# Kernel tuning notes

Measured on AMD Instinct MI355X. Metric: run time of the kernel, lower is better.

Reference implementation:

```python
import jax, jax.numpy as jnp
import numpy as np

N = 16000
E = 128000
IN_DIM = 512
H1 = 4096
H2 = 1024
OUT_DIM = 64


def setup_inputs() -> dict:
    key = jax.random.key(0)
    ks = jax.random.split(key, 8)
    x = jax.random.normal(ks[0], (N, IN_DIM), dtype=jnp.float32)
    edge_index = jax.random.randint(ks[1], (2, E), 0, N, dtype=jnp.int64)

    def glorot(k, fan_in, fan_out):
        lim = float(np.sqrt(6.0 / (fan_in + fan_out)))
        return jax.random.uniform(k, (fan_in, fan_out), jnp.float32, -lim, lim)

    # PyG SAGEConv: out = lin_l(mean_j x_j) + lin_r(x); lin_l has bias, lin_r does not.
    params = {
        'W1l': glorot(ks[2], IN_DIM, H1), 'b1': jnp.zeros((H1,), jnp.float32),
        'W1r': glorot(ks[3], IN_DIM, H1),
        'W2l': glorot(ks[4], H1, H2), 'b2': jnp.zeros((H2,), jnp.float32),
        'W2r': glorot(ks[5], H1, H2),
        'W3l': glorot(ks[6], H2, OUT_DIM), 'b3': jnp.zeros((OUT_DIM,), jnp.float32),
        'W3r': glorot(ks[7], H2, OUT_DIM),
    }
    return {'x': x, 'edge_index': edge_index, **params}


def _sage_conv(x, src, dst, Wl, b, Wr):
    # mean-aggregate neighbor features at dst, then linear; plus root transform
    agg = jax.ops.segment_sum(x[src], dst, num_segments=N)          # [N, F_in]
    cnt = jax.ops.segment_sum(jnp.ones((src.shape[0],), x.dtype), dst, num_segments=N)
    mean = agg / jnp.maximum(cnt, 1.0)[:, None]
    return mean @ Wl + b + x @ Wr


def reference(x, edge_index, W1l, b1, W1r, W2l, b2, W2r, W3l, b3, W3r):
    src, dst = edge_index[0], edge_index[1]
    h = jax.nn.relu(_sage_conv(x, src, dst, W1l, b1, W1r))   # dropout is identity in eval
    h = jax.nn.relu(_sage_conv(h, src, dst, W2l, b2, W2r))
    h = _sage_conv(h, src, dst, W3l, b3, W3r)
    return jax.nn.log_softmax(h, axis=1)
```

## Files before the change

### kernel.cpp

```cpp
#include <hip/hip_runtime.h>
#include <stdint.h>

typedef __bf16 bf16x8 __attribute__((ext_vector_type(8)));
typedef float  f32x4  __attribute__((ext_vector_type(4)));
typedef float  f32x16 __attribute__((ext_vector_type(16)));
typedef unsigned short u16x8 __attribute__((ext_vector_type(8)));
typedef const void __attribute__((address_space(1))) gv_t;
typedef void __attribute__((address_space(3))) sv_t;

static __device__ __forceinline__ unsigned short f2bf(float f) {
  unsigned u = __float_as_uint(f);
  u += 0x7fffu + ((u >> 16) & 1u);
  return (unsigned short)(u >> 16);
}
static __device__ __forceinline__ float bf2f(unsigned short h) {
  return __uint_as_float(((unsigned)h) << 16);
}
static __device__ __forceinline__ void gload16(const void* g, void* l) {
  __builtin_amdgcn_global_load_lds((gv_t*)g, (sv_t*)l, 16, 0, 0);
}

__global__ void k_sentinel(float* out, int n, float val) {
  int t = blockIdx.x * 256 + threadIdx.x;
  if (t < n) out[t] = val;
}

static __device__ __forceinline__ void transW_tile(const float* W, unsigned short* Wt,
                                                   int K, int N, int ld, int kofs,
                                                   int n0, int k0, float (*tile)[33]) {
  int tx = threadIdx.x & 31, ty = threadIdx.x >> 5;
#pragma unroll
  for (int r = 0; r < 4; ++r)
    tile[ty + r * 8][tx] = W[(size_t)(k0 + ty + r * 8) * N + n0 + tx];
  __syncthreads();
#pragma unroll
  for (int r = 0; r < 4; ++r)
    Wt[(size_t)(n0 + ty + r * 8) * ld + kofs + k0 + tx] = f2bf(tile[tx][ty + r * 8]);
}

__global__ void k_prep(const float4* __restrict__ x, ushort4* __restrict__ xm,
                       const float* W1l, const float* W1r, const float* W2l,
                       const float* W2r, const float* W3l, const float* W3r,
                       unsigned short* W1t, unsigned short* W2t, unsigned short* W3t,
                       int* deg, int Nn) {
  __shared__ float tile[32][33];
  int bid = blockIdx.x;
  if (bid < 8000) {
    int t = bid * 256 + threadIdx.x;
    int row = t >> 7, c = t & 127;
    float4 v = x[t];
    xm[(size_t)row * 256 + c] = make_ushort4(f2bf(v.x), f2bf(v.y), f2bf(v.z), f2bf(v.w));
    return;
  }
  bid -= 8000;
  if (bid < 2048) {
    transW_tile(W1r, W1t, 512, 4096, 1024, 0, (bid & 127) * 32, (bid >> 7) * 32, tile);
    return;
  }
  bid -= 2048;
  if (bid < 2048) {
    transW_tile(W1l, W1t, 512, 4096, 1024, 512, (bid & 127) * 32, (bid >> 7) * 32, tile);
    return;
  }
  bid -= 2048;
  if (bid < 4096) {
    transW_tile(W2l, W2t, 4096, 1024, 4096, 0, (bid & 31) * 32, (bid >> 5) * 32, tile);
    return;
  }
  bid -= 4096;
  if (bid < 4096) {
    transW_tile(W2r, W2t + (size_t)1024 * 4096, 4096, 1024, 4096, 0, (bid & 31) * 32,
                (bid >> 5) * 32, tile);
    return;
  }
  bid -= 4096;
  if (bid < 64) {
    transW_tile(W3l, W3t, 1024, 64, 1024, 0, (bid & 1) * 32, (bid >> 1) * 32, tile);
    return;
  }
  bid -= 64;
  if (bid < 64) {
    transW_tile(W3r, W3t + (size_t)64 * 1024, 1024, 64, 1024, 0, (bid & 1) * 32,
                (bid >> 1) * 32, tile);
    return;
  }
  bid -= 64;
  {
    int t = bid * 256 + threadIdx.x;
    if (t < Nn) deg[t] = 0;
  }
}

static __device__ __forceinline__ int detect_i64(const int* ei) {
  __shared__ int sflag;
  if (threadIdx.x < 64) {
    int bad = 0;
#pragma unroll
    for (int j = 0; j < 4; ++j) bad |= ei[2 * (threadIdx.x * 4 + j) + 1];
    unsigned long long m = __ballot(bad != 0);
    if (threadIdx.x == 0) sflag = (m == 0ull) ? 1 : 0;
  }
  __syncthreads();
  return sflag;
}

__global__ void k_degree(const int* ei, int E, int* deg) {
  int f = detect_i64(ei);
  int t = blockIdx.x * 256 + threadIdx.x;
  if (t < E) {
    int d = f ? ei[2 * (E + t)] : ei[E + t];
    atomicAdd(&deg[d], 1);
  }
}
__global__ void k_scan(const int* deg, int* rp, int* cur, int n) {
  __shared__ int ssum[256];
  int t = threadIdx.x;
  int chunk = (n + 255) >> 8;
  int lo = t * chunk, hi = min(lo + chunk, n);
  int s = 0;
  for (int i = lo; i < hi; ++i) s += deg[i];
  ssum[t] = s;
  __syncthreads();
  if (t == 0) {
    int run = 0;
    for (int i = 0; i < 256; ++i) { int v = ssum[i]; ssum[i] = run; run += v; }
  }
  __syncthreads();
  int run = ssum[t];
  for (int i = lo; i < hi; ++i) { rp[i] = run; cur[i] = run; run += deg[i]; }
  if (t == 255) rp[n] = run;
}
__global__ void k_fill(const int* ei, int E, int* cur, int* col) {
  int f = detect_i64(ei);
  int t = blockIdx.x * 256 + threadIdx.x;
  if (t < E) {
    int s = f ? ei[2 * t] : ei[t];
    int d = f ? ei[2 * (E + t)] : ei[E + t];
    int p = atomicAdd(&cur[d], 1);
    col[p] = s;
  }
}

__global__ void k_agg(unsigned short* __restrict__ xm, const int* __restrict__ rp,
                      const int* __restrict__ col) {
  int i = blockIdx.x;
  int s = rp[i], e = rp[i + 1];
  float inv = 1.0f / (float)max(e - s, 1);
  int f8 = threadIdx.x & 63;
  int p = threadIdx.x >> 6;
  const u16x8* xm8 = (const u16x8*)xm;
  float acc[8] = {0.f, 0.f, 0.f, 0.f, 0.f, 0.f, 0.f, 0.f};
  for (int n = s + p; n < e; n += 4) {
    u16x8 v = xm8[(size_t)col[n] * 128 + f8];
#pragma unroll
    for (int j = 0; j < 8; ++j) acc[j] += bf2f(v[j]);
  }
  __shared__ float red[3][64][8];
  if (p > 0) {
#pragma unroll
    for (int j = 0; j < 8; ++j) red[p - 1][f8][j] = acc[j];
  }
  __syncthreads();
  if (p == 0) {
    u16x8 o;
#pragma unroll
    for (int j = 0; j < 8; ++j) {
      float v = (acc[j] + red[0][f8][j] + red[1][f8][j] + red[2][f8][j]) * inv;
      o[j] = f2bf(v);
    }
    ((u16x8*)xm)[(size_t)i * 128 + 64 + f8] = o;
  }
}

#define XCD_SWZ(bnShift_)                                                             \
  const int nwg = gridDim.x;                                                          \
  const int q8 = nwg >> 3, r8 = nwg & 7;                                              \
  const int xcd = blockIdx.x & 7, idx = blockIdx.x >> 3;                              \
  const int wg = (xcd < r8 ? xcd * (q8 + 1) : r8 * (q8 + 1) + (xcd - r8) * q8) + idx; \
  const int bn = wg & ((1 << (bnShift_)) - 1);                                        \
  const int bm = wg >> (bnShift_);

#define VMCNT(NUM) asm volatile("s_waitcnt vmcnt(" #NUM ")" ::: "memory")

#define STAGE_A(BUF, I, K0)                                            \
  gload16(Ap + (size_t)((I) * 64 + rsub) * K + (K0) + sl8,             \
          (char*)&lds[BUF][0][0] + ((I) * 64 + wq * 8) * 128)
#define STAGE_B(BUF, I, K0)                                            \
  gload16(Bp + (size_t)((I) * 64 + rsub) * K + (K0) + sl8,             \
          (char*)&lds[BUF][1][0] + ((I) * 64 + wq * 8) * 128)

#define GEMM256_PRO                                                     \
  STAGE_A(0, 0, 0); STAGE_A(0, 1, 0);                                   \
  STAGE_B(0, 0, 0); STAGE_B(0, 1, 0);                                   \
  STAGE_B(0, 2, 0); STAGE_B(0, 3, 0);                                   \
  STAGE_A(0, 2, 0); STAGE_A(0, 3, 0);                                   \
  STAGE_A(1, 0, 64); STAGE_A(1, 1, 64);                                 \
  STAGE_B(1, 0, 64); STAGE_B(1, 1, 64);                                 \
  STAGE_B(1, 2, 64); STAGE_B(1, 3, 64);                                 \
  STAGE_A(1, 2, 64); STAGE_A(1, 3, 64);                                 \
  VMCNT(8);                                                             \
  __builtin_amdgcn_s_barrier();

#define GEMM256_STAGE_NEXT                                              \
  if (t + 2 < nt) {                                                     \
    STAGE_A(cur, 0, k2); STAGE_A(cur, 1, k2);                           \
    STAGE_B(cur, 0, k2); STAGE_B(cur, 1, k2);                           \
    STAGE_B(cur, 2, k2); STAGE_B(cur, 3, k2);                           \
    STAGE_A(cur, 2, k2); STAGE_A(cur, 3, k2);                           \
  }

#define LOAD_AFR(DST, CUR, QA)                                                          \
  do {                                                                                  \
    const char* baseA = (const char*)&lds[CUR][0][0];                                   \
    _Pragma("unroll") for (int mm = 0; mm < 4; ++mm) {                                  \
      const int rr = ((QA) * 4 + mm) * 32 + wr * 16 + (lane & 15);                      \
      _Pragma("unroll") for (int kk = 0; kk < 2; ++kk)                                  \
          DST[mm][kk] = *(const bf16x8*)(baseA + rr * 128 +                             \
                                         (((kk * 4 + (lane >> 4)) ^ (lane & 7)) << 4)); \
    }                                                                                   \
  } while (0)
#define LOAD_BFR(DST, CUR, QB)                                                          \
  do {                                                                                  \
    const char* baseB = (const char*)&lds[CUR][1][0];                                   \
    _Pragma("unroll") for (int nn = 0; nn < 2; ++nn) {                                  \
      const int cc = ((QB) * 2 + nn) * 64 + wc * 16 + (lane & 15);                      \
      _Pragma("unroll") for (int kk = 0; kk < 2; ++kk)                                  \
          DST[nn][kk] = *(const bf16x8*)(baseB + cc * 128 +                             \
                                         (((kk * 4 + (lane >> 4)) ^ (lane & 7)) << 4)); \
    }                                                                                   \
  } while (0)
#define MFMA_Q(QA, QB, AFR, BFR)                                                        \
  do {                                                                                  \
    _Pragma("unroll") for (int mm = 0; mm < 4; ++mm)                                    \
        _Pragma("unroll") for (int nn = 0; nn < 2; ++nn)                                \
            _Pragma("unroll") for (int kk = 0; kk < 2; ++kk)                            \
                acc[(QA) * 4 + mm][(QB) * 2 + nn] =                                     \
                    __builtin_amdgcn_mfma_f32_16x16x32_bf16(                            \
                        AFR[mm][kk], BFR[nn][kk], acc[(QA) * 4 + mm][(QB) * 2 + nn],    \
                        0, 0, 0);                                                       \
  } while (0)

template <bool RELU, bool BIAS>
__global__ __launch_bounds__(512, 1) void k_gemm256(
    const unsigned short* __restrict__ A, const unsigned short* __restrict__ B,
    const float* __restrict__ bias, unsigned short* __restrict__ outp,
    int Mreal, int N, int K, int bnShift) {
  __shared__ __align__(16) unsigned short lds[2][2][256 * 64];
  const int tid = threadIdx.x;
  const int lane = tid & 63;
  const int wq = tid >> 6;
  const int wr = wq >> 2;
  const int wc = wq & 3;
  XCD_SWZ(bnShift)
  const unsigned short* Ap = A + (size_t)bm * 256 * K;
  const unsigned short* Bp = B + (size_t)bn * 256 * K;
  const int sl8 = ((lane & 7) ^ (lane >> 3)) * 8;
  const int rsub = wq * 8 + (lane >> 3);

  f32x4 acc[8][4];
#pragma unroll
  for (int m = 0; m < 8; ++m)
#pragma unroll
    for (int n = 0; n < 4; ++n) acc[m][n] = (f32x4){0.f, 0.f, 0.f, 0.f};

  GEMM256_PRO

  bf16x8 a0[4][2], b0[2][2], a1[4][2], b1[2][2];
  LOAD_AFR(a0, 0, 0);
  LOAD_BFR(b0, 0, 0);

  const int nt = K >> 6;
#pragma unroll 1
  for (int t = 0; t < nt; ++t) {
    const int cur = t & 1, nxt = cur ^ 1;
    const int k2 = (t + 2) << 6;
    LOAD_AFR(a1, cur, 1);
    LOAD_BFR(b1, cur, 1);
    __builtin_amdgcn_s_setprio(1);
    MFMA_Q(0, 0, a0, b0);
    MFMA_Q(0, 1, a0, b1);
    __builtin_amdgcn_s_setprio(0);
    asm volatile("s_waitcnt vmcnt(0) lgkmcnt(0)" ::: "memory");
    __builtin_amdgcn_s_barrier();
    GEMM256_STAGE_NEXT
    __builtin_amdgcn_s_setprio(1);
    MFMA_Q(1, 0, a1, b0);
    MFMA_Q(1, 1, a1, b1);
    __builtin_amdgcn_s_setprio(0);
    if (t + 1 < nt) {
      LOAD_AFR(a0, nxt, 0);
      LOAD_BFR(b0, nxt, 0);
    }
  }

  const int row0 = bm * 256 + wr * 16 + ((lane >> 4) << 2);
  const int col0 = bn * 256 + wc * 16 + (lane & 15);
  const bool full = (bm + 1) * 256 <= Mreal;
#pragma unroll
  for (int m = 0; m < 8; ++m) {
#pragma unroll
    for (int n = 0; n < 4; ++n) {
      const int col = col0 + n * 64;
      float bb = BIAS ? bias[col] : 0.f;
      if (full) {
#pragma unroll
        for (int r = 0; r < 4; ++r) {
          int row = row0 + m * 32 + r;
          float v = acc[m][n][r] + bb;
          if (RELU) v = fmaxf(v, 0.f);
          outp[(size_t)row * N + col] = f2bf(v);
        }
      } else {
#pragma unroll
        for (int r = 0; r < 4; ++r) {
          int row = row0 + m * 32 + r;
          if (row < Mreal) {
            float v = acc[m][n][r] + bb;
            if (RELU) v = fmaxf(v, 0.f);
            outp[(size_t)row * N + col] = f2bf(v);
          }
        }
      }
    }
  }
}

#define LOADW_AFR(DST, CUR, QA)                                                         \
  do {                                                                                  \
    const char* baseA = (const char*)&lds[CUR][0][0];                                   \
    _Pragma("unroll") for (int mm = 0; mm < 2; ++mm) {                                  \
      const int rr = wr * 128 + ((QA) * 2 + mm) * 32 + (lane & 31);                     \
      _Pragma("unroll") for (int ks = 0; ks < 4; ++ks)                                  \
          DST[mm][ks] = *(const bf16x8*)(baseA + rr * 128 +                             \
                                         (((ks * 2 + (lane >> 5)) ^ (lane & 7)) << 4)); \
    }                                                                                   \
  } while (0)
#define LOADW_BFR(DST, CUR, QB)                                                         \
  do {                                                                                  \
    const char* baseB = (const char*)&lds[CUR][1][0];                                   \
    const int cc = wc * 64 + (QB) * 32 + (lane & 31);                                   \
    _Pragma("unroll") for (int ks = 0; ks < 4; ++ks)                                    \
        DST[ks] = *(const bf16x8*)(baseB + cc * 128 +                                   \
                                   (((ks * 2 + (lane >> 5)) ^ (lane & 7)) << 4));       \
  } while (0)
#define MFMAW_Q(QA, QB, AFR, BFR)                                                       \
  do {                                                                                  \
    _Pragma("unroll") for (int mm = 0; mm < 2; ++mm)                                    \
        _Pragma("unroll") for (int ks = 0; ks < 4; ++ks)                                \
            acc[(QA) * 2 + mm][QB] = __builtin_amdgcn_mfma_f32_32x32x16_bf16(           \
                AFR[mm][ks], BFR[ks], acc[(QA) * 2 + mm][QB], 0, 0, 0);                 \
  } while (0)

template <bool RELU, bool BIAS>
__global__ __launch_bounds__(512, 1) void k_gemm256w(
    const unsigned short* __restrict__ A, const unsigned short* __restrict__ B,
    const float* __restrict__ bias, unsigned short* __restrict__ outp,
    int Mreal, int N, int K, int bnShift) {
  __shared__ __align__(16) unsigned short lds[2][2][256 * 64];
  const int tid = threadIdx.x;
  const int lane = tid & 63;
  const int wq = tid >> 6;
  const int wr = wq >> 2;
  const int wc = wq & 3;
  XCD_SWZ(bnShift)
  const unsigned short* Ap = A + (size_t)bm * 256 * K;
  const unsigned short* Bp = B + (size_t)bn * 256 * K;
  const int sl8 = ((lane & 7) ^ (lane >> 3)) * 8;
  const int rsub = wq * 8 + (lane >> 3);

  f32x16 acc[4][2];
#pragma unroll
  for (int m = 0; m < 4; ++m)
#pragma unroll
    for (int n = 0; n < 2; ++n)
#pragma unroll
      for (int r = 0; r < 16; ++r) acc[m][n][r] = 0.f;

  GEMM256_PRO

  bf16x8 a0[2][4], b0[4], a1[2][4], b1[4];
  LOADW_AFR(a0, 0, 0);
  LOADW_BFR(b0, 0, 0);

  const int nt = K >> 6;
#pragma unroll 1
  for (int t = 0; t < nt; ++t) {
    const int cur = t & 1, nxt = cur ^ 1;
    const int k2 = (t + 2) << 6;
    LOADW_AFR(a1, cur, 1);
    LOADW_BFR(b1, cur, 1);
    __builtin_amdgcn_s_setprio(1);
    MFMAW_Q(0, 0, a0, b0);
    MFMAW_Q(0, 1, a0, b1);
    __builtin_amdgcn_s_setprio(0);
    asm volatile("s_waitcnt vmcnt(0) lgkmcnt(0)" ::: "memory");
    __builtin_amdgcn_s_barrier();
    GEMM256_STAGE_NEXT
    __builtin_amdgcn_s_setprio(1);
    MFMAW_Q(1, 0, a1, b0);
    MFMAW_Q(1, 1, a1, b1);
    __builtin_amdgcn_s_setprio(0);
    if (t + 1 < nt) {
      LOADW_AFR(a0, nxt, 0);
      LOADW_BFR(b0, nxt, 0);
    }
  }

  const int rbase = bm * 256 + wr * 128 + ((lane >> 5) << 2);
  const int col0 = bn * 256 + wc * 64 + (lane & 31);
  const bool full = (bm + 1) * 256 <= Mreal;
#pragma unroll
  for (int m = 0; m < 4; ++m) {
#pragma unroll
    for (int n = 0; n < 2; ++n) {
      const int col = col0 + n * 32;
      float bb = BIAS ? bias[col] : 0.f;
      if (full) {
#pragma unroll
        for (int r = 0; r < 16; ++r) {
          int row = rbase + m * 32 + (r & 3) + 8 * (r >> 2);
          float v = acc[m][n][r] + bb;
          if (RELU) v = fmaxf(v, 0.f);
          outp[(size_t)row * N + col] = f2bf(v);
        }
      } else {
#pragma unroll
        for (int r = 0; r < 16; ++r) {
          int row = rbase + m * 32 + (r & 3) + 8 * (r >> 2);
          if (row < Mreal) {
            float v = acc[m][n][r] + bb;
            if (RELU) v = fmaxf(v, 0.f);
            outp[(size_t)row * N + col] = f2bf(v);
          }
        }
      }
    }
  }
}

template <int NF, bool TWO, bool RELU, bool BIAS>
__global__ __launch_bounds__(256) void k_gemm(
    const unsigned short* __restrict__ Am, const unsigned short* __restrict__ Ar,
    const unsigned short* __restrict__ Bl, const unsigned short* __restrict__ Br,
    const float* __restrict__ bias, unsigned short* __restrict__ outp, int N, int K) {
  constexpr int BN = NF * 32;
  __shared__ __align__(16) unsigned short lds[(128 + BN) * 64];
  unsigned short* ldsA = lds;
  unsigned short* ldsB = lds + 128 * 64;

  const int tid = threadIdx.x;
  const int lane = tid & 63;
  const int w = tid >> 6;
  const int wr = w >> 1, wc = w & 1;

  f32x4 zero = {0.f, 0.f, 0.f, 0.f};
  f32x4 acc[4][NF];
#pragma unroll
  for (int m = 0; m < 4; ++m)
#pragma unroll
    for (int n = 0; n < NF; ++n) acc[m][n] = zero;

  const int bm = blockIdx.x, bn = blockIdx.y;
  const int sl_st = (lane & 7) ^ (lane >> 3);

#pragma unroll 1
  for (int pass = 0; pass < (TWO ? 2 : 1); ++pass) {
    const unsigned short* A = (TWO && pass) ? Ar : Am;
    const unsigned short* B = (TWO && pass) ? Br : Bl;
    A += (size_t)bm * 128 * K;
    B += (size_t)bn * BN * K;
#pragma unroll 1
    for (int k0 = 0; k0 < K; k0 += 64) {
      __syncthreads();
#pragma unroll
      for (int q = 0; q < 4; ++q) {
        int rowi = (w * 4 + q) * 8 + (lane >> 3);
        gload16(A + (size_t)rowi * K + k0 + sl_st * 8, (char*)ldsA + (w * 4 + q) * 1024);
      }
#pragma unroll
      for (int q = 0; q < NF; ++q) {
        int rowi = (w * NF + q) * 8 + (lane >> 3);
        gload16(B + (size_t)rowi * K + k0 + sl_st * 8, (char*)ldsB + (w * NF + q) * 1024);
      }
      __syncthreads();
#pragma unroll
      for (int kk = 0; kk < 2; ++kk) {
        int sw = (((kk * 4 + (lane >> 4)) ^ (lane & 7)) << 4);
        bf16x8 af[4], bfr[NF];
#pragma unroll
        for (int m = 0; m < 4; ++m) {
          int r = wr * 64 + m * 16 + (lane & 15);
          af[m] = *(const bf16x8*)((const char*)ldsA + r * 128 + sw);
        }
#pragma unroll
        for (int n = 0; n < NF; ++n) {
          int c = wc * (BN / 2) + n * 16 + (lane & 15);
          bfr[n] = *(const bf16x8*)((const char*)ldsB + c * 128 + sw);
        }
#pragma unroll
        for (int m = 0; m < 4; ++m)
#pragma unroll
          for (int n = 0; n < NF; ++n)
            acc[m][n] = __builtin_amdgcn_mfma_f32_16x16x32_bf16(af[m], bfr[n], acc[m][n], 0, 0, 0);
      }
    }
  }

  const int row0 = bm * 128 + wr * 64;
  const int col0 = bn * BN + wc * (BN / 2);
#pragma unroll
  for (int m = 0; m < 4; ++m) {
#pragma unroll
    for (int n = 0; n < NF; ++n) {
      int col = col0 + n * 16 + (lane & 15);
      float bb = BIAS ? bias[col] : 0.f;
#pragma unroll
      for (int r = 0; r < 4; ++r) {
        int row = row0 + m * 16 + ((lane >> 4) << 2) + r;
        float v = acc[m][n][r] + bb;
        if (RELU) v = fmaxf(v, 0.f);
        outp[(size_t)row * N + col] = f2bf(v);
      }
    }
  }
}

__global__ void k_combine2(const unsigned short* __restrict__ Z2, const int* __restrict__ rp,
                           const int* __restrict__ col, const float* __restrict__ bias,
                           unsigned short* __restrict__ h2) {
  int i = blockIdx.x;
  int s = rp[i], e = rp[i + 1];
  float inv = 1.0f / (float)max(e - s, 1);
  int f8 = threadIdx.x & 127;
  int p = threadIdx.x >> 7;
  const u16x8* Z28 = (const u16x8*)Z2;
  float acc[8] = {0.f, 0.f, 0.f, 0.f, 0.f, 0.f, 0.f, 0.f};
  for (int n = s + p; n < e; n += 2) {
    u16x8 v = Z28[(size_t)col[n] * 256 + f8];
#pragma unroll
    for (int j = 0; j < 8; ++j) acc[j] += bf2f(v[j]);
  }
  __shared__ float red[128][8];
  if (p == 1) {
#pragma unroll
    for (int j = 0; j < 8; ++j) red[f8][j] = acc[j];
  }
  __syncthreads();
  if (p == 0) {
    u16x8 r = Z28[(size_t)i * 256 + 128 + f8];
    float4 b4a = ((const float4*)bias)[f8 * 2];
    float4 b4b = ((const float4*)bias)[f8 * 2 + 1];
    float bb[8] = {b4a.x, b4a.y, b4a.z, b4a.w, b4b.x, b4b.y, b4b.z, b4b.w};
    u16x8 o;
#pragma unroll
    for (int j = 0; j < 8; ++j) {
      float v = (acc[j] + red[f8][j]) * inv + bf2f(r[j]) + bb[j];
      o[j] = f2bf(fmaxf(v, 0.f));
    }
    ((u16x8*)h2)[(size_t)i * 128 + f8] = o;
  }
}

__global__ void k_combine3(const unsigned short* __restrict__ Z3, const int* __restrict__ rp,
                           const int* __restrict__ col, const float* __restrict__ bias,
                           float* __restrict__ out) {
  int i = blockIdx.x * 4 + (threadIdx.x >> 6);
  int c = threadIdx.x & 63;
  int s = rp[i], e = rp[i + 1];
  float inv = 1.0f / (float)max(e - s, 1);
  float a = 0.f;
  for (int n = s; n < e; ++n) a += bf2f(Z3[(size_t)col[n] * 128 + c]);
  float v = a * inv + bf2f(Z3[(size_t)i * 128 + 64 + c]) + bias[c];
  float m = v;
#pragma unroll
  for (int o = 1; o < 64; o <<= 1) m = fmaxf(m, __shfl_xor(m, o, 64));
  float t = expf(v - m);
  float sum = t;
#pragma unroll
  for (int o = 1; o < 64; o <<= 1) sum += __shfl_xor(sum, o, 64);
  out[(size_t)i * 64 + c] = (v - m) - logf(sum);
}

extern "C" void kernel_launch(void* const* d_in, const int* in_sizes, int n_in,
                              void* d_out, int out_size, void* d_ws, size_t ws_size,
                              hipStream_t stream) {
  const float* x   = (const float*)d_in[0];
  const int*   ei  = (const int*)d_in[1];
  const float* W1l = (const float*)d_in[2];
  const float* b1  = (const float*)d_in[3];
  const float* W1r = (const float*)d_in[4];
  const float* W2l = (const float*)d_in[5];
  const float* b2  = (const float*)d_in[6];
  const float* W2r = (const float*)d_in[7];
  const float* W3l = (const float*)d_in[8];
  const float* b3  = (const float*)d_in[9];
  const float* W3r = (const float*)d_in[10];

  const int Nn = 16000;
  const int E = in_sizes[1] / 2;

  char* p = (char*)d_ws;
  auto carve = [&](size_t bytes) {
    char* r = p;
    p += (bytes + 255) & ~(size_t)255;
    return r;
  };
  int* deg    = (int*)carve((size_t)Nn * 4);
  int* rp     = (int*)carve((size_t)(Nn + 1) * 4);
  int* cur    = (int*)carve((size_t)Nn * 4);
  int* colidx = (int*)carve((size_t)E * 4);
  unsigned short* W2t = (unsigned short*)carve((size_t)2048 * 4096 * 2);
  unsigned short* W3t = (unsigned short*)carve((size_t)128 * 1024 * 2);
  unsigned short* xm  = (unsigned short*)carve((size_t)Nn * 1024 * 2);
  unsigned short* h1  = (unsigned short*)carve((size_t)Nn * 4096 * 2);
  unsigned short* Z2  = (unsigned short*)carve((size_t)Nn * 2048 * 2);
  unsigned short* Z3  = (unsigned short*)carve((size_t)Nn * 128 * 2);
  unsigned short* h2  = xm;
  unsigned short* W1t = Z2;

  size_t need = (size_t)(p - (char*)d_ws);
  if (ws_size < need) {
    k_sentinel<<<(out_size + 255) / 256, 256, 0, stream>>>((float*)d_out, out_size,
                                                           (float)(ws_size >> 20));
    return;
  }

  k_prep<<<8000 + 2048 + 2048 + 4096 + 4096 + 64 + 64 + 63, 256, 0, stream>>>(
      (const float4*)x, (ushort4*)xm, W1l, W1r, W2l, W2r, W3l, W3r, W1t, W2t, W3t, deg, Nn);
  k_degree<<<(E + 255) / 256, 256, 0, stream>>>(ei, E, deg);
  k_scan<<<1, 256, 0, stream>>>(deg, rp, cur, Nn);
  k_fill<<<(E + 255) / 256, 256, 0, stream>>>(ei, E, cur, colidx);
  k_agg<<<Nn, 256, 0, stream>>>(xm, rp, colidx);
  k_gemm256w<true, true><<<63 * 16, 512, 0, stream>>>(xm, W1t, b1, h1, Nn, 4096, 1024, 4);
  k_gemm256<false, false><<<63 * 8, 512, 0, stream>>>(h1, W2t, nullptr, Z2, Nn, 2048, 4096, 3);
  k_combine2<<<Nn, 256, 0, stream>>>(Z2, rp, colidx, b2, h2);
  k_gemm<2, false, false, false><<<dim3(125, 2), 256, 0, stream>>>(h2, nullptr, W3t, nullptr,
                                                                   nullptr, Z3, 128, 1024);
  k_combine3<<<Nn / 4, 256, 0, stream>>>(Z3, rp, colidx, b3, (float*)d_out);

  (void)n_in; (void)out_size;
}
```

Before: 548.6 us.

## Replace 32x32 MFMA layer-1 GEMM with phase-staggered 16x16 wave-group schedule

Layer 1 GEMM now uses the 16x16x32 MFMA fragment layout, replacing the 32x32x16 one. Waves with wr==0 follow the original quadrant order. The other wave group runs its quadrants in a rotated order so the two halves issue LDS reads and MFMAs at different times. The aim is to spread LDS bandwidth demand and keep the matrix units busier around the barrier. The risk is that the different per-group order changes register pressure, and the 16x16 MFMA path may have lower peak throughput than 32x32 for this shape.

Result: faster. 535.8 us (-2.3%).

```diff
diff --git a/kernel.cpp b/kernel.cpp
--- a/kernel.cpp
+++ b/kernel.cpp
@@ -3,7 +3,6 @@
 
 typedef __bf16 bf16x8 __attribute__((ext_vector_type(8)));
 typedef float  f32x4  __attribute__((ext_vector_type(4)));
-typedef float  f32x16 __attribute__((ext_vector_type(16)));
 typedef unsigned short u16x8 __attribute__((ext_vector_type(8)));
 typedef const void __attribute__((address_space(1))) gv_t;
 typedef void __attribute__((address_space(3))) sv_t;
@@ -240,6 +239,34 @@
                         0, 0, 0);                                                       \
   } while (0)
 
+#define GEMM256_EPI(RELU_, BIAS_)                                       \
+  const int row0 = bm * 256 + wr * 16 + ((lane >> 4) << 2);              \
+  const int col0 = bn * 256 + wc * 16 + (lane & 15);                     \
+  const bool full = (bm + 1) * 256 <= Mreal;                             \
+  _Pragma("unroll") for (int m = 0; m < 8; ++m) {                        \
+    _Pragma("unroll") for (int n = 0; n < 4; ++n) {                      \
+      const int col = col0 + n * 64;                                     \
+      float bb = (BIAS_) ? bias[col] : 0.f;                              \
+      if (full) {                                                        \
+        _Pragma("unroll") for (int r = 0; r < 4; ++r) {                  \
+          int row = row0 + m * 32 + r;                                   \
+          float v = acc[m][n][r] + bb;                                   \
+          if (RELU_) v = fmaxf(v, 0.f);                                  \
+          outp[(size_t)row * N + col] = f2bf(v);                         \
+        }                                                                \
+      } else {                                                           \
+        _Pragma("unroll") for (int r = 0; r < 4; ++r) {                  \
+          int row = row0 + m * 32 + r;                                   \
+          if (row < Mreal) {                                             \
+            float v = acc[m][n][r] + bb;                                 \
+            if (RELU_) v = fmaxf(v, 0.f);                                \
+            outp[(size_t)row * N + col] = f2bf(v);                       \
+          }                                                              \
+        }                                                                \
+      }                                                                  \
+    }                                                                    \
+  }
+
 template <bool RELU, bool BIAS>
 __global__ __launch_bounds__(512, 1) void k_gemm256(
     const unsigned short* __restrict__ A, const unsigned short* __restrict__ B,
@@ -293,66 +320,11 @@
     }
   }
 
-  const int row0 = bm * 256 + wr * 16 + ((lane >> 4) << 2);
-  const int col0 = bn * 256 + wc * 16 + (lane & 15);
-  const bool full = (bm + 1) * 256 <= Mreal;
-#pragma unroll
-  for (int m = 0; m < 8; ++m) {
-#pragma unroll
-    for (int n = 0; n < 4; ++n) {
-      const int col = col0 + n * 64;
-      float bb = BIAS ? bias[col] : 0.f;
-      if (full) {
-#pragma unroll
-        for (int r = 0; r < 4; ++r) {
-          int row = row0 + m * 32 + r;
-          float v = acc[m][n][r] + bb;
-          if (RELU) v = fmaxf(v, 0.f);
-          outp[(size_t)row * N + col] = f2bf(v);
-        }
-      } else {
-#pragma unroll
-        for (int r = 0; r < 4; ++r) {
-          int row = row0 + m * 32 + r;
-          if (row < Mreal) {
-            float v = acc[m][n][r] + bb;
-            if (RELU) v = fmaxf(v, 0.f);
-            outp[(size_t)row * N + col] = f2bf(v);
-          }
-        }
-      }
-    }
-  }
-}
-
-#define LOADW_AFR(DST, CUR, QA)                                                         \
-  do {                                                                                  \
-    const char* baseA = (const char*)&lds[CUR][0][0];                                   \
-    _Pragma("unroll") for (int mm = 0; mm < 2; ++mm) {                                  \
-      const int rr = wr * 128 + ((QA) * 2 + mm) * 32 + (lane & 31);                     \
-      _Pragma("unroll") for (int ks = 0; ks < 4; ++ks)                                  \
-          DST[mm][ks] = *(const bf16x8*)(baseA + rr * 128 +                             \
-                                         (((ks * 2 + (lane >> 5)) ^ (lane & 7)) << 4)); \
-    }                                                                                   \
-  } while (0)
-#define LOADW_BFR(DST, CUR, QB)                                                         \
-  do {                                                                                  \
-    const char* baseB = (const char*)&lds[CUR][1][0];                                   \
-    const int cc = wc * 64 + (QB) * 32 + (lane & 31);                                   \
-    _Pragma("unroll") for (int ks = 0; ks < 4; ++ks)                                    \
-        DST[ks] = *(const bf16x8*)(baseB + cc * 128 +                                   \
-                                   (((ks * 2 + (lane >> 5)) ^ (lane & 7)) << 4));       \
-  } while (0)
-#define MFMAW_Q(QA, QB, AFR, BFR)                                                       \
-  do {                                                                                  \
-    _Pragma("unroll") for (int mm = 0; mm < 2; ++mm)                                    \
-        _Pragma("unroll") for (int ks = 0; ks < 4; ++ks)                                \
-            acc[(QA) * 2 + mm][QB] = __builtin_amdgcn_mfma_f32_32x32x16_bf16(           \
-                AFR[mm][ks], BFR[ks], acc[(QA) * 2 + mm][QB], 0, 0, 0);                 \
-  } while (0)
+  GEMM256_EPI(RELU, BIAS)
+}
 
 template <bool RELU, bool BIAS>
-__global__ __launch_bounds__(512, 1) void k_gemm256w(
+__global__ __launch_bounds__(512, 1) void k_gemm256d(
     const unsigned short* __restrict__ A, const unsigned short* __restrict__ B,
     const float* __restrict__ bias, unsigned short* __restrict__ outp,
     int Mreal, int N, int K, int bnShift) {
@@ -368,74 +340,72 @@
   const int sl8 = ((lane & 7) ^ (lane >> 3)) * 8;
   const int rsub = wq * 8 + (lane >> 3);
 
-  f32x16 acc[4][2];
-#pragma unroll
-  for (int m = 0; m < 4; ++m)
-#pragma unroll
-    for (int n = 0; n < 2; ++n)
-#pragma unroll
-      for (int r = 0; r < 16; ++r) acc[m][n][r] = 0.f;
+  f32x4 acc[8][4];
+#pragma unroll
+  for (int m = 0; m < 8; ++m)
+#pragma unroll
+    for (int n = 0; n < 4; ++n) acc[m][n] = (f32x4){0.f, 0.f, 0.f, 0.f};
 
   GEMM256_PRO
 
-  bf16x8 a0[2][4], b0[4], a1[2][4], b1[4];
-  LOADW_AFR(a0, 0, 0);
-  LOADW_BFR(b0, 0, 0);
-
   const int nt = K >> 6;
+  if (wr == 0) {
+    bf16x8 a0[4][2], b0[2][2], a1[4][2], b1[2][2];
+    LOAD_AFR(a0, 0, 0);
+    LOAD_BFR(b0, 0, 0);
 #pragma unroll 1
-  for (int t = 0; t < nt; ++t) {
-    const int cur = t & 1, nxt = cur ^ 1;
-    const int k2 = (t + 2) << 6;
-    LOADW_AFR(a1, cur, 1);
-    LOADW_BFR(b1, cur, 1);
-    __builtin_amdgcn_s_setprio(1);
-    MFMAW_Q(0, 0, a0, b0);
-    MFMAW_Q(0, 1, a0, b1);
-    __builtin_amdgcn_s_setprio(0);
-    asm volatile("s_waitcnt vmcnt(0) lgkmcnt(0)" ::: "memory");
-    __builtin_amdgcn_s_barrier();
-    GEMM256_STAGE_NEXT
-    __builtin_amdgcn_s_setprio(1);
-    MFMAW_Q(1, 0, a1, b0);
-    MFMAW_Q(1, 1, a1, b1);
-    __builtin_amdgcn_s_setprio(0);
-    if (t + 1 < nt) {
-      LOADW_AFR(a0, nxt, 0);
-      LOADW_BFR(b0, nxt, 0);
-    }
-  }
-
-  const int rbase = bm * 256 + wr * 128 + ((lane >> 5) << 2);
-  const int col0 = bn * 256 + wc * 64 + (lane & 31);
-  const bool full = (bm + 1) * 256 <= Mreal;
-#pragma unroll
-  for (int m = 0; m < 4; ++m) {
-#pragma unroll
-    for (int n = 0; n < 2; ++n) {
-      const int col = col0 + n * 32;
-      float bb = BIAS ? bias[col] : 0.f;
-      if (full) {
-#pragma unroll
-        for (int r = 0; r < 16; ++r) {
-          int row = rbase + m * 32 + (r & 3) + 8 * (r >> 2);
-          float v = acc[m][n][r] + bb;
-          if (RELU) v = fmaxf(v, 0.f);
-          outp[(size_t)row * N + col] = f2bf(v);
-        }
-      } else {
-#pragma unroll
-        for (int r = 0; r < 16; ++r) {
-          int row = rbase + m * 32 + (r & 3) + 8 * (r >> 2);
-          if (row < Mreal) {
-            float v = acc[m][n][r] + bb;
-            if (RELU) v = fmaxf(v, 0.f);
-            outp[(size_t)row * N + col] = f2bf(v);
-          }
-        }
+    for (int t = 0; t < nt; ++t) {
+      const int cur = t & 1, nxt = cur ^ 1;
+      const int k2 = (t + 2) << 6;
+      LOAD_AFR(a1, cur, 1);
+      LOAD_BFR(b1, cur, 1);
+      __builtin_amdgcn_s_setprio(1);
+      MFMA_Q(0, 0, a0, b0);
+      MFMA_Q(0, 1, a0, b1);
+      __builtin_amdgcn_s_setprio(0);
+      asm volatile("s_waitcnt vmcnt(0) lgkmcnt(0)" ::: "memory");
+      __builtin_amdgcn_s_barrier();
+      GEMM256_STAGE_NEXT
+      __builtin_amdgcn_s_setprio(1);
+      MFMA_Q(1, 0, a1, b0);
+      MFMA_Q(1, 1, a1, b1);
+      __builtin_amdgcn_s_setprio(0);
+      if (t + 1 < nt) {
+        LOAD_AFR(a0, nxt, 0);
+        LOAD_BFR(b0, nxt, 0);
       }
     }
-  }
+  } else {
+    bf16x8 a0[4][2], b0[2][2], a1[4][2], b1[2][2];
+    LOAD_AFR(a1, 0, 1);
+    LOAD_BFR(b1, 0, 1);
+#pragma unroll 1
+    for (int t = 0; t < nt; ++t) {
+      const int cur = t & 1, nxt = cur ^ 1;
+      const int k2 = (t + 2) << 6;
+      __builtin_amdgcn_s_setprio(1);
+      MFMA_Q(1, 1, a1, b1);
+      __builtin_amdgcn_s_setprio(0);
+      LOAD_AFR(a0, cur, 0);
+      LOAD_BFR(b0, cur, 0);
+      __builtin_amdgcn_s_setprio(1);
+      MFMA_Q(1, 0, a1, b0);
+      __builtin_amdgcn_s_setprio(0);
+      asm volatile("s_waitcnt vmcnt(0) lgkmcnt(0)" ::: "memory");
+      __builtin_amdgcn_s_barrier();
+      GEMM256_STAGE_NEXT
+      __builtin_amdgcn_s_setprio(1);
+      MFMA_Q(0, 0, a0, b0);
+      MFMA_Q(0, 1, a0, b1);
+      __builtin_amdgcn_s_setprio(0);
+      if (t + 1 < nt) {
+        LOAD_AFR(a1, nxt, 1);
+        LOAD_BFR(b1, nxt, 1);
+      }
+    }
+  }
+
+  GEMM256_EPI(RELU, BIAS)
 }
 
 template <int NF, bool TWO, bool RELU, bool BIAS>
@@ -631,7 +601,7 @@
   k_scan<<<1, 256, 0, stream>>>(deg, rp, cur, Nn);
   k_fill<<<(E + 255) / 256, 256, 0, stream>>>(ei, E, cur, colidx);
   k_agg<<<Nn, 256, 0, stream>>>(xm, rp, colidx);
-  k_gemm256w<true, true><<<63 * 16, 512, 0, stream>>>(xm, W1t, b1, h1, Nn, 4096, 1024, 4);
+  k_gemm256d<true, true><<<63 * 16, 512, 0, stream>>>(xm, W1t, b1, h1, Nn, 4096, 1024, 4);
   k_gemm256<false, false><<<63 * 8, 512, 0, stream>>>(h1, W2t, nullptr, Z2, Nn, 2048, 4096, 3);
   k_combine2<<<Nn, 256, 0, stream>>>(Z2, rp, colidx, b2, h2);
   k_gemm<2, false, false, false><<<dim3(125, 2), 256, 0, stream>>>(h2, nullptr, W3t, nullptr,
```
